# Kernel optimization log

Measured on AMD Instinct MI355X. Metric: run time of the kernel, lower is better.

## Reference

```python
import jax, jax.numpy as jnp
import numpy as np

N_NODES = 100000


def gcn_conv(x, src, dst, W, b, n):
    # PyG GCNConv: add self-loops (weight 1), symmetric deg^-1/2 normalization,
    # linear transform, scatter-add to targets, then bias.
    loop = jnp.arange(n, dtype=src.dtype)
    s = jnp.concatenate([src, loop])
    d = jnp.concatenate([dst, loop])
    w = jnp.ones(s.shape[0], dtype=x.dtype)
    deg = jax.ops.segment_sum(w, d, num_segments=n)
    dis = jnp.where(deg > 0, jax.lax.rsqrt(deg), 0.0)
    norm = dis[s] * w * dis[d]                      # [E+N]
    h = x @ W                                       # [N, out]
    msg = h[s] * norm[:, None]                      # [E+N, out]
    out = jax.ops.segment_sum(msg, d, num_segments=n)
    return out + b


def setup_inputs() -> dict:
    key = jax.random.key(0)
    ks = jax.random.split(key, 8)
    num_node_types, emb_dim, hidden_dim, out_dim = 1000, 128, 128, 64
    n, e = N_NODES, 1600000
    x_node_types = jax.random.randint(ks[0], (n,), 0, num_node_types, dtype=jnp.int64 if jax.config.jax_enable_x64 else jnp.int32)
    edge_index = jax.random.randint(ks[1], (2, e), 0, n, dtype=x_node_types.dtype)
    emb = jax.random.normal(ks[2], (num_node_types, emb_dim), dtype=jnp.float32)
    W1 = jax.random.normal(ks[3], (emb_dim, hidden_dim), dtype=jnp.float32) / np.sqrt(emb_dim)
    b1 = jnp.zeros((hidden_dim,), dtype=jnp.float32)
    W2 = jax.random.normal(ks[4], (hidden_dim, out_dim), dtype=jnp.float32) / np.sqrt(hidden_dim)
    b2 = jnp.zeros((out_dim,), dtype=jnp.float32)
    return {"x_node_types": x_node_types, "edge_index": edge_index,
            "emb": emb, "W1": W1, "b1": b1, "W2": W2, "b2": b2}


def reference(x_node_types, edge_index, emb, W1, b1, W2, b2):
    n = N_NODES
    src, dst = edge_index[0], edge_index[1]
    x = emb[x_node_types]                           # embedding lookup [N, emb_dim]
    x = jax.nn.relu(gcn_conv(x, src, dst, W1, b1, n))
    # dropout p=0.5 is identity in eval mode (training=False)
    x = gcn_conv(x, src, dst, W2, b2, n)
    return x
```

## Files before the change

kernel.cpp:

```cpp
#include <hip/hip_runtime.h>
#include <hip/hip_bf16.h>


#define D1 128
#define D2 64
#define BSH 9
#define BW  512
#define BMAX 256
#define TILE 2048

typedef __attribute__((ext_vector_type(8))) short short8v;
typedef __attribute__((ext_vector_type(4))) float f32x4;

__device__ __forceinline__ short bf16_hi(float x) {
    return (short)(__float_as_uint(x) >> 16);
}
__device__ __forceinline__ float hi_f(float x) {
    return __uint_as_float(__float_as_uint(x) & 0xFFFF0000u);
}
__device__ __forceinline__ short bf16_rne(float x) {
    unsigned u = __float_as_uint(x);
    return (short)((u + 0x7FFFu + ((u >> 16) & 1u)) >> 16);
}

__global__ __launch_bounds__(256) void bhist_k(const int* __restrict__ dst,
                                               int* __restrict__ bcnt, int e) {
    __shared__ int h[BMAX];
    if (threadIdx.x < BMAX) h[threadIdx.x] = 0;
    __syncthreads();
    int stride = gridDim.x * blockDim.x;
    for (int t = blockIdx.x * blockDim.x + threadIdx.x; t < e; t += stride)
        atomicAdd(&h[dst[t] >> BSH], 1);
    __syncthreads();
    if (threadIdx.x < BMAX && h[threadIdx.x])
        atomicAdd(&bcnt[threadIdx.x], h[threadIdx.x]);
}

__global__ void bscan_k(const int* __restrict__ bcnt, int* __restrict__ bbase,
                        int* __restrict__ bcur, int nb) {
    __shared__ int tmp[BMAX];
    int tid = threadIdx.x;
    int v = (tid < nb) ? bcnt[tid] : 0;
    tmp[tid] = v;
    __syncthreads();
    for (int s = 1; s < BMAX; s <<= 1) {
        int a = (tid >= s) ? tmp[tid - s] : 0;
        __syncthreads();
        tmp[tid] += a;
        __syncthreads();
    }
    if (tid < nb) { int ex = tmp[tid] - v; bbase[tid] = ex; bcur[tid] = ex; }
}

__global__ __launch_bounds__(256) void bpart_k(const int* __restrict__ src,
                                               const int* __restrict__ dst,
                                               int* __restrict__ bcur,
                                               int2* __restrict__ ebuf, int e) {
    __shared__ int hist[BMAX];
    __shared__ int chunk[BMAX];
    __shared__ int lcur[BMAX];
    int tid = threadIdx.x;
    int base = blockIdx.x * TILE;
    if (tid < BMAX) { hist[tid] = 0; lcur[tid] = 0; }
    __syncthreads();
    int s8[8], d8[8], b8[8];
    #pragma unroll
    for (int i = 0; i < 8; ++i) {
        int t = base + i * 256 + tid;
        if (t < e) {
            s8[i] = src[t]; d8[i] = dst[t]; b8[i] = d8[i] >> BSH;
            atomicAdd(&hist[b8[i]], 1);
        } else b8[i] = -1;
    }
    __syncthreads();
    if (tid < BMAX && hist[tid]) chunk[tid] = atomicAdd(&bcur[tid], hist[tid]);
    __syncthreads();
    #pragma unroll
    for (int i = 0; i < 8; ++i) {
        if (b8[i] >= 0) {
            int r = atomicAdd(&lcur[b8[i]], 1);
            ebuf[chunk[b8[i]] + r] = make_int2(s8[i], d8[i]);
        }
    }
}

__global__ __launch_bounds__(512) void bcsr_k(const int2* __restrict__ ebuf,
                                              const int* __restrict__ bbase,
                                              const int* __restrict__ bcnt,
                                              const int* __restrict__ types,
                                              int* __restrict__ cnt,
                                              int* __restrict__ off,
                                              int2* __restrict__ csr, int n) {
    __shared__ int lcnt[BW];
    __shared__ int lsc[BW];
    __shared__ int lcur[BW];
    int b = blockIdx.x;
    int d0 = b << BSH;
    int tid = threadIdx.x;
    lcnt[tid] = 0; lcur[tid] = 0;
    __syncthreads();
    int ebase = bbase[b], ecnt = bcnt[b];
    for (int t = tid; t < ecnt; t += BW)
        atomicAdd(&lcnt[ebuf[ebase + t].y - d0], 1);
    __syncthreads();
    int v = lcnt[tid];
    lsc[tid] = v;
    __syncthreads();
    for (int s = 1; s < BW; s <<= 1) {
        int a = (tid >= s) ? lsc[tid - s] : 0;
        __syncthreads();
        lsc[tid] += a;
        __syncthreads();
    }
    int ex = lsc[tid] - v;
    int node = d0 + tid;
    if (node < n) { cnt[node] = v; off[node] = ebase + ex; }
    __syncthreads();
    lsc[tid] = ex;
    __syncthreads();
    for (int t = tid; t < ecnt; t += BW) {
        int2 q = ebuf[ebase + t];
        int l = q.y - d0;
        int r = atomicAdd(&lcur[l], 1);
        csr[ebase + lsc[l] + r] = make_int2(q.x, types[q.x]);
    }
}

__global__ void dis_k(const int* __restrict__ cnt, float* __restrict__ dis, int n) {
    int stride = gridDim.x * blockDim.x;
    for (int t = blockIdx.x * blockDim.x + threadIdx.x; t < n; t += stride)
        dis[t] = rsqrtf((float)(cnt[t] + 1));
}

__global__ void w2prep_k(const float* __restrict__ W2,
                         short* __restrict__ w2h, short* __restrict__ w2l) {
    int t = blockIdx.x * blockDim.x + threadIdx.x;
    if (t >= D1 * D2) return;
    int k = t >> 6, c = t & 63;
    float v = W2[t];
    int ct = c >> 4, kb = k >> 5;
    int l = (((k >> 3) & 3) << 4) | (c & 15);
    int j = k & 7;
    int idx = (((ct << 2) | kb) * 64 + l) * 8 + j;
    w2h[idx] = bf16_hi(v);
    w2l[idx] = bf16_rne(v - hi_f(v));
}

__global__ __launch_bounds__(128) void gemm_emb_k(const float* __restrict__ emb,
                                                  const float* __restrict__ W1,
                                                  float* __restrict__ embW, int ntypes) {
    __shared__ float w[D1 * D1];
    for (int t = threadIdx.x; t < D1 * D1; t += 128) w[t] = W1[t];
    __syncthreads();
    int j = threadIdx.x;
    for (int r = blockIdx.x; r < ntypes; r += gridDim.x) {
        const float* er = emb + (size_t)r * D1;
        float acc = 0.f;
        #pragma unroll 8
        for (int k = 0; k < D1; ++k) acc = fmaf(er[k], w[k * D1 + j], acc);
        embW[(size_t)r * D1 + j] = acc;
    }
}

__global__ __launch_bounds__(256) void agg1_k(const int* __restrict__ types,
                                              const int2* __restrict__ csr,
                                              const int* __restrict__ off,
                                              const int* __restrict__ cnt,
                                              const float* __restrict__ dis,
                                              const float* __restrict__ embW,
                                              const float* __restrict__ b1,
                                              float* __restrict__ x1, int n) {
    int i = (blockIdx.x * blockDim.x + threadIdx.x) >> 6;
    if (i >= n) return;
    int lane = threadIdx.x & 63;
    int sub = lane >> 5;
    int fl = (lane & 31) << 2;
    float disi = dis[i];
    int ti = types[i];
    int base = off[i], c = cnt[i];
    int total = c + 1;
    float4 acc = make_float4(0.f, 0.f, 0.f, 0.f);
    for (int cb = 0; cb < total; cb += 64) {
        int idx = cb + lane;
        int t_l = 0;
        float c_l = 0.f;
        if (idx < c) {
            int2 q = csr[base + idx];
            t_l = q.y;
            c_l = disi * dis[q.x];
        } else if (idx == c) {
            t_l = ti;
            c_l = disi * disi;
        }
        int m = min(64, total - cb);
        for (int k0 = 0; k0 < m; k0 += 2) {
            int k = k0 + sub;
            int t = __shfl(t_l, k);
            float cf = __shfl(c_l, k);
            float4 v = *(const float4*)(embW + (size_t)t * D1 + fl);
            acc.x = fmaf(v.x, cf, acc.x);
            acc.y = fmaf(v.y, cf, acc.y);
            acc.z = fmaf(v.z, cf, acc.z);
            acc.w = fmaf(v.w, cf, acc.w);
        }
    }
    acc.x += __shfl_xor(acc.x, 32);
    acc.y += __shfl_xor(acc.y, 32);
    acc.z += __shfl_xor(acc.z, 32);
    acc.w += __shfl_xor(acc.w, 32);
    if (sub == 0) {
        float4 bv = ((const float4*)b1)[lane & 31];
        acc.x = fmaxf(acc.x + bv.x, 0.f);
        acc.y = fmaxf(acc.y + bv.y, 0.f);
        acc.z = fmaxf(acc.z + bv.z, 0.f);
        acc.w = fmaxf(acc.w + bv.w, 0.f);
        ((float4*)(x1 + (size_t)i * D1))[lane & 31] = acc;
    }
}

__global__ __launch_bounds__(256) void gemm2_k(float* __restrict__ x1,
                                               const short* __restrict__ w2h,
                                               const short* __restrict__ w2l, int n) {
    int gw = (blockIdx.x * blockDim.x + threadIdx.x) >> 6;
    int lane = threadIdx.x & 63;
    int r0 = gw << 4;
    if (r0 >= n) return;
    int row = r0 + (lane & 15);
    int kq = lane >> 4;
    bool ok = row < n;
    const float* xr = x1 + (size_t)row * D1 + kq * 8;
    short8v ah[4], al[4];
    #pragma unroll
    for (int kb = 0; kb < 4; ++kb) {
        float4 v0, v1;
        if (ok) {
            v0 = *(const float4*)(xr + kb * 32);
            v1 = *(const float4*)(xr + kb * 32 + 4);
        } else {
            v0 = make_float4(0.f, 0.f, 0.f, 0.f);
            v1 = v0;
        }
        float xv[8] = {v0.x, v0.y, v0.z, v0.w, v1.x, v1.y, v1.z, v1.w};
        #pragma unroll
        for (int j = 0; j < 8; ++j) {
            ah[kb][j] = bf16_hi(xv[j]);
            al[kb][j] = bf16_rne(xv[j] - hi_f(xv[j]));
        }
    }
    const short8v* w2hv = (const short8v*)w2h;
    const short8v* w2lv = (const short8v*)w2l;
    #pragma unroll
    for (int ct = 0; ct < 4; ++ct) {
        f32x4 acc = {0.f, 0.f, 0.f, 0.f};
        #pragma unroll
        for (int kb = 0; kb < 4; ++kb) {
            short8v bh = w2hv[(ct * 4 + kb) * 64 + lane];
            short8v bl = w2lv[(ct * 4 + kb) * 64 + lane];
            acc = __builtin_amdgcn_mfma_f32_16x16x32_bf16(ah[kb], bh, acc, 0, 0, 0);
            acc = __builtin_amdgcn_mfma_f32_16x16x32_bf16(al[kb], bh, acc, 0, 0, 0);
            acc = __builtin_amdgcn_mfma_f32_16x16x32_bf16(ah[kb], bl, acc, 0, 0, 0);
        }
        #pragma unroll
        for (int v = 0; v < 4; ++v) {
            int orow = r0 + (lane >> 4) * 4 + v;
            if (orow < n)
                x1[(size_t)orow * D1 + ct * 16 + (lane & 15)] = acc[v];
        }
    }
}

__global__ __launch_bounds__(256) void agg2_k(const int2* __restrict__ csr,
                                              const int* __restrict__ off,
                                              const int* __restrict__ cnt,
                                              const float* __restrict__ dis,
                                              const float* __restrict__ h2,
                                              const float* __restrict__ b2,
                                              float* __restrict__ out, int n) {
    int i = (blockIdx.x * blockDim.x + threadIdx.x) >> 6;
    if (i >= n) return;
    int lane = threadIdx.x & 63;
    int sub = lane >> 4;
    int fl = (lane & 15) << 2;
    float disi = dis[i];
    int base = off[i], c = cnt[i];
    int total = c + 1;
    float4 acc = make_float4(0.f, 0.f, 0.f, 0.f);
    for (int cb = 0; cb < total; cb += 64) {
        int idx = cb + lane;
        int s_l = i;
        float c_l = 0.f;
        if (idx < c) {
            int2 q = csr[base + idx];
            s_l = q.x;
            c_l = disi * dis[q.x];
        } else if (idx == c) {
            c_l = disi * disi;
        }
        int m = min(64, total - cb);
        for (int k0 = 0; k0 < m; k0 += 4) {
            int k = k0 + sub;
            int s = __shfl(s_l, k);
            float cf = __shfl(c_l, k);
            float4 v = *(const float4*)(h2 + (size_t)s * D1 + fl);
            acc.x = fmaf(v.x, cf, acc.x);
            acc.y = fmaf(v.y, cf, acc.y);
            acc.z = fmaf(v.z, cf, acc.z);
            acc.w = fmaf(v.w, cf, acc.w);
        }
    }
    acc.x += __shfl_xor(acc.x, 16);
    acc.y += __shfl_xor(acc.y, 16);
    acc.z += __shfl_xor(acc.z, 16);
    acc.w += __shfl_xor(acc.w, 16);
    acc.x += __shfl_xor(acc.x, 32);
    acc.y += __shfl_xor(acc.y, 32);
    acc.z += __shfl_xor(acc.z, 32);
    acc.w += __shfl_xor(acc.w, 32);
    if (sub == 0) {
        float4 bv = ((const float4*)b2)[lane & 15];
        acc.x += bv.x;
        acc.y += bv.y;
        acc.z += bv.z;
        acc.w += bv.w;
        ((float4*)(out + (size_t)i * D2))[lane & 15] = acc;
    }
}

extern "C" void kernel_launch(void* const* d_in, const int* in_sizes, int n_in,
                              void* d_out, int out_size, void* d_ws, size_t ws_size,
                              hipStream_t stream) {
    const int* types = (const int*)d_in[0];
    const int* edges = (const int*)d_in[1];
    const float* emb = (const float*)d_in[2];
    const float* W1  = (const float*)d_in[3];
    const float* b1  = (const float*)d_in[4];
    const float* W2  = (const float*)d_in[5];
    const float* b2  = (const float*)d_in[6];
    float* out = (float*)d_out;

    const int n = in_sizes[0];
    const int e = in_sizes[1] / 2;
    const int ntypes = in_sizes[2] / D1;
    const int* src = edges;
    const int* dst = edges + e;
    const int nb = (n + BW - 1) >> BSH;

    char* p = (char*)d_ws;
    auto alloc = [&](size_t bytes) {
        char* r = p;
        p += (bytes + 255) & ~(size_t)255;
        return r;
    };
    int*   bcnt  = (int*)  alloc(BMAX * 4);
    int*   bbase = (int*)  alloc(BMAX * 4);
    int*   bcur  = (int*)  alloc(BMAX * 4);
    int*   cnt   = (int*)  alloc((size_t)n * 4);
    int*   off   = (int*)  alloc((size_t)n * 4);
    float* dis   = (float*)alloc((size_t)n * 4);
    short* w2h   = (short*)alloc((size_t)D1 * D2 * 2);
    short* w2l   = (short*)alloc((size_t)D1 * D2 * 2);
    int2*  ebuf  = (int2*) alloc((size_t)e * 8);
    int2*  csr   = (int2*) alloc((size_t)e * 8);
    float* embW  = (float*)alloc((size_t)ntypes * D1 * 4);
    float* x1    = (float*)alloc((size_t)n * D1 * 4);
    (void)ws_size;

    hipMemsetAsync(bcnt, 0, BMAX * 4, stream);

    bhist_k<<<512, 256, 0, stream>>>(dst, bcnt, e);
    bscan_k<<<1, BMAX, 0, stream>>>(bcnt, bbase, bcur, nb);
    bpart_k<<<(e + TILE - 1) / TILE, 256, 0, stream>>>(src, dst, bcur, ebuf, e);
    bcsr_k<<<nb, BW, 0, stream>>>(ebuf, bbase, bcnt, types, cnt, off, csr, n);
    dis_k<<<(n + 255) / 256, 256, 0, stream>>>(cnt, dis, n);
    w2prep_k<<<(D1 * D2 + 255) / 256, 256, 0, stream>>>(W2, w2h, w2l);

    gemm_emb_k<<<256, 128, 0, stream>>>(emb, W1, embW, ntypes);
    int nwb = (n + 3) / 4;
    agg1_k<<<nwb, 256, 0, stream>>>(types, csr, off, cnt, dis, embW, b1, x1, n);

    int ngw = (n + 15) / 16;
    gemm2_k<<<(ngw + 3) / 4, 256, 0, stream>>>(x1, w2h, w2l, n);
    agg2_k<<<nwb, 256, 0, stream>>>(csr, off, cnt, dis, x1, b2, out, n);
}
```

Before: 310.6 us.

## Pack edge records into 32-bit words and store layer-2 features as bf16

Edge records in the partition buffer and the CSR are packed into single 32-bit words: 17 bits of source index plus either the local destination slot or the node type. This halves the bytes written and read by the partition, CSR build and aggregation passes. The second-layer transformed features are now written as bf16 into a dense n×64 buffer instead of fp32 with row stride 128, which cuts the gather traffic in agg2. The cost is lower precision in layer 2, and the packing assumes node and type ids fit in 17 and 15 bits.

New measurement: 293.7 us. 1.06x faster.

```diff
diff --git a/kernel.cpp b/kernel.cpp
--- a/kernel.cpp
+++ b/kernel.cpp
@@ -8,6 +8,7 @@
 #define BW  512
 #define BMAX 256
 #define TILE 2048
+#define SMASK 0x1FFFF
 
 typedef __attribute__((ext_vector_type(8))) short short8v;
 typedef __attribute__((ext_vector_type(4))) float f32x4;
@@ -21,6 +22,9 @@
 __device__ __forceinline__ short bf16_rne(float x) {
     unsigned u = __float_as_uint(x);
     return (short)((u + 0x7FFFu + ((u >> 16) & 1u)) >> 16);
+}
+__device__ __forceinline__ float bf16_f(unsigned short u) {
+    return __uint_as_float((unsigned)u << 16);
 }
 
 __global__ __launch_bounds__(256) void bhist_k(const int* __restrict__ dst,
@@ -55,7 +59,7 @@
 __global__ __launch_bounds__(256) void bpart_k(const int* __restrict__ src,
                                                const int* __restrict__ dst,
                                                int* __restrict__ bcur,
-                                               int2* __restrict__ ebuf, int e) {
+                                               unsigned* __restrict__ ebuf, int e) {
     __shared__ int hist[BMAX];
     __shared__ int chunk[BMAX];
     __shared__ int lcur[BMAX];
@@ -63,12 +67,15 @@
     int base = blockIdx.x * TILE;
     if (tid < BMAX) { hist[tid] = 0; lcur[tid] = 0; }
     __syncthreads();
-    int s8[8], d8[8], b8[8];
+    unsigned p8[8];
+    int b8[8];
     #pragma unroll
     for (int i = 0; i < 8; ++i) {
         int t = base + i * 256 + tid;
         if (t < e) {
-            s8[i] = src[t]; d8[i] = dst[t]; b8[i] = d8[i] >> BSH;
+            int s = src[t], d = dst[t];
+            b8[i] = d >> BSH;
+            p8[i] = (unsigned)s | ((unsigned)(d & (BW - 1)) << 17);
             atomicAdd(&hist[b8[i]], 1);
         } else b8[i] = -1;
     }
@@ -79,18 +86,18 @@
     for (int i = 0; i < 8; ++i) {
         if (b8[i] >= 0) {
             int r = atomicAdd(&lcur[b8[i]], 1);
-            ebuf[chunk[b8[i]] + r] = make_int2(s8[i], d8[i]);
-        }
-    }
-}
-
-__global__ __launch_bounds__(512) void bcsr_k(const int2* __restrict__ ebuf,
+            ebuf[chunk[b8[i]] + r] = p8[i];
+        }
+    }
+}
+
+__global__ __launch_bounds__(512) void bcsr_k(const unsigned* __restrict__ ebuf,
                                               const int* __restrict__ bbase,
                                               const int* __restrict__ bcnt,
                                               const int* __restrict__ types,
                                               int* __restrict__ cnt,
                                               int* __restrict__ off,
-                                              int2* __restrict__ csr, int n) {
+                                              unsigned* __restrict__ csr, int n) {
     __shared__ int lcnt[BW];
     __shared__ int lsc[BW];
     __shared__ int lcur[BW];
@@ -101,7 +108,7 @@
     __syncthreads();
     int ebase = bbase[b], ecnt = bcnt[b];
     for (int t = tid; t < ecnt; t += BW)
-        atomicAdd(&lcnt[ebuf[ebase + t].y - d0], 1);
+        atomicAdd(&lcnt[ebuf[ebase + t] >> 17], 1);
     __syncthreads();
     int v = lcnt[tid];
     lsc[tid] = v;
@@ -119,10 +126,11 @@
     lsc[tid] = ex;
     __syncthreads();
     for (int t = tid; t < ecnt; t += BW) {
-        int2 q = ebuf[ebase + t];
-        int l = q.y - d0;
+        unsigned q = ebuf[ebase + t];
+        int l = q >> 17;
+        int s = q & SMASK;
         int r = atomicAdd(&lcur[l], 1);
-        csr[ebase + lsc[l] + r] = make_int2(q.x, types[q.x]);
+        csr[ebase + lsc[l] + r] = (unsigned)s | ((unsigned)types[s] << 17);
     }
 }
 
@@ -163,7 +171,7 @@
 }
 
 __global__ __launch_bounds__(256) void agg1_k(const int* __restrict__ types,
-                                              const int2* __restrict__ csr,
+                                              const unsigned* __restrict__ csr,
                                               const int* __restrict__ off,
                                               const int* __restrict__ cnt,
                                               const float* __restrict__ dis,
@@ -185,9 +193,9 @@
         int t_l = 0;
         float c_l = 0.f;
         if (idx < c) {
-            int2 q = csr[base + idx];
-            t_l = q.y;
-            c_l = disi * dis[q.x];
+            unsigned q = csr[base + idx];
+            t_l = q >> 17;
+            c_l = disi * dis[q & SMASK];
         } else if (idx == c) {
             t_l = ti;
             c_l = disi * disi;
@@ -218,9 +226,10 @@
     }
 }
 
-__global__ __launch_bounds__(256) void gemm2_k(float* __restrict__ x1,
+__global__ __launch_bounds__(256) void gemm2_k(const float* __restrict__ x1,
                                                const short* __restrict__ w2h,
-                                               const short* __restrict__ w2l, int n) {
+                                               const short* __restrict__ w2l,
+                                               unsigned short* __restrict__ h2b, int n) {
     int gw = (blockIdx.x * blockDim.x + threadIdx.x) >> 6;
     int lane = threadIdx.x & 63;
     int r0 = gw << 4;
@@ -264,16 +273,17 @@
         for (int v = 0; v < 4; ++v) {
             int orow = r0 + (lane >> 4) * 4 + v;
             if (orow < n)
-                x1[(size_t)orow * D1 + ct * 16 + (lane & 15)] = acc[v];
-        }
-    }
-}
-
-__global__ __launch_bounds__(256) void agg2_k(const int2* __restrict__ csr,
+                h2b[(size_t)orow * D2 + ct * 16 + (lane & 15)] =
+                    (unsigned short)bf16_rne(acc[v]);
+        }
+    }
+}
+
+__global__ __launch_bounds__(256) void agg2_k(const unsigned* __restrict__ csr,
                                               const int* __restrict__ off,
                                               const int* __restrict__ cnt,
                                               const float* __restrict__ dis,
-                                              const float* __restrict__ h2,
+                                              const unsigned short* __restrict__ h2b,
                                               const float* __restrict__ b2,
                                               float* __restrict__ out, int n) {
     int i = (blockIdx.x * blockDim.x + threadIdx.x) >> 6;
@@ -290,9 +300,9 @@
         int s_l = i;
         float c_l = 0.f;
         if (idx < c) {
-            int2 q = csr[base + idx];
-            s_l = q.x;
-            c_l = disi * dis[q.x];
+            unsigned q = csr[base + idx];
+            s_l = q & SMASK;
+            c_l = disi * dis[s_l];
         } else if (idx == c) {
             c_l = disi * disi;
         }
@@ -301,11 +311,11 @@
             int k = k0 + sub;
             int s = __shfl(s_l, k);
             float cf = __shfl(c_l, k);
-            float4 v = *(const float4*)(h2 + (size_t)s * D1 + fl);
-            acc.x = fmaf(v.x, cf, acc.x);
-            acc.y = fmaf(v.y, cf, acc.y);
-            acc.z = fmaf(v.z, cf, acc.z);
-            acc.w = fmaf(v.w, cf, acc.w);
+            ushort4 hv = *(const ushort4*)(h2b + (size_t)s * D2 + fl);
+            acc.x = fmaf(bf16_f(hv.x), cf, acc.x);
+            acc.y = fmaf(bf16_f(hv.y), cf, acc.y);
+            acc.z = fmaf(bf16_f(hv.z), cf, acc.z);
+            acc.w = fmaf(bf16_f(hv.w), cf, acc.w);
         }
     }
     acc.x += __shfl_xor(acc.x, 16);
@@ -351,18 +361,19 @@
         p += (bytes + 255) & ~(size_t)255;
         return r;
     };
-    int*   bcnt  = (int*)  alloc(BMAX * 4);
-    int*   bbase = (int*)  alloc(BMAX * 4);
-    int*   bcur  = (int*)  alloc(BMAX * 4);
-    int*   cnt   = (int*)  alloc((size_t)n * 4);
-    int*   off   = (int*)  alloc((size_t)n * 4);
-    float* dis   = (float*)alloc((size_t)n * 4);
-    short* w2h   = (short*)alloc((size_t)D1 * D2 * 2);
-    short* w2l   = (short*)alloc((size_t)D1 * D2 * 2);
-    int2*  ebuf  = (int2*) alloc((size_t)e * 8);
-    int2*  csr   = (int2*) alloc((size_t)e * 8);
-    float* embW  = (float*)alloc((size_t)ntypes * D1 * 4);
-    float* x1    = (float*)alloc((size_t)n * D1 * 4);
+    int*      bcnt  = (int*)      alloc(BMAX * 4);
+    int*      bbase = (int*)      alloc(BMAX * 4);
+    int*      bcur  = (int*)      alloc(BMAX * 4);
+    int*      cnt   = (int*)      alloc((size_t)n * 4);
+    int*      off   = (int*)      alloc((size_t)n * 4);
+    float*    dis   = (float*)    alloc((size_t)n * 4);
+    short*    w2h   = (short*)    alloc((size_t)D1 * D2 * 2);
+    short*    w2l   = (short*)    alloc((size_t)D1 * D2 * 2);
+    unsigned* ebuf  = (unsigned*) alloc((size_t)e * 4);
+    unsigned* csr   = (unsigned*) alloc((size_t)e * 4);
+    float*    embW  = (float*)    alloc((size_t)ntypes * D1 * 4);
+    float*    x1    = (float*)    alloc((size_t)n * D1 * 4);
+    unsigned short* h2b = (unsigned short*)alloc((size_t)n * D2 * 2);
     (void)ws_size;
 
     hipMemsetAsync(bcnt, 0, BMAX * 4, stream);
@@ -379,6 +390,6 @@
     agg1_k<<<nwb, 256, 0, stream>>>(types, csr, off, cnt, dis, embW, b1, x1, n);
 
     int ngw = (n + 15) / 16;
-    gemm2_k<<<(ngw + 3) / 4, 256, 0, stream>>>(x1, w2h, w2l, n);
-    agg2_k<<<nwb, 256, 0, stream>>>(csr, off, cnt, dis, x1, b2, out, n);
-}
+    gemm2_k<<<(ngw + 3) / 4, 256, 0, stream>>>(x1, w2h, w2l, h2b, n);
+    agg2_k<<<nwb, 256, 0, stream>>>(csr, off, cnt, dis, h2b, b2, out, n);
+}
```
